# Kernel tuning notes

Measured on AMD Instinct MI355X. Metric: run time of the kernel, lower is better.

Reference implementation:

```python
import jax, jax.numpy as jnp
import numpy as np

WS = 6      # window_size
SS = 3      # shift_size
NH = 8      # num_heads
DIM = 384
HD = DIM // NH
SCALE = HD ** -0.5


def _window_mask(H, W):
    # region ids: [:ss,:ss]=0, [:ss,ss:]=1, [ss:,:ss]=2, [ss:,ss:]=3
    row = (jnp.arange(H) >= SS).astype(jnp.int32)
    col = (jnp.arange(W) >= SS).astype(jnp.int32)
    region = row[:, None] * 2 + col[None, :]            # (H, W)
    region = jnp.roll(region, (-SS, -SS), axis=(0, 1))
    ids = region.reshape(H // WS, WS, W // WS, WS).transpose(0, 2, 1, 3)
    ids = ids.reshape(-1, WS * WS)                      # (nW, V)
    eq = ids[:, :, None] == ids[:, None, :]             # (nW, V, V)
    return jnp.where(eq, 0.0, -jnp.inf).astype(jnp.float32)


def setup_inputs():
    key = jax.random.key(0)
    k = jax.random.split(key, 5)
    B, H, W, D = 32, 48, 48, DIM
    return {
        "x": jax.random.normal(k[0], (B, H, W, D), jnp.float32),
        "w_qkv": jax.random.normal(k[1], (D, 3 * D), jnp.float32) * 0.02,
        "b_qkv": jax.random.normal(k[2], (3 * D,), jnp.float32) * 0.02,
        "w_proj": jax.random.normal(k[3], (D, D), jnp.float32) * 0.02,
        "b_proj": jax.random.normal(k[4], (D,), jnp.float32) * 0.02,
    }


def reference(x, w_qkv, b_qkv, w_proj, b_proj):
    B, H, W, D = x.shape
    nWh, nWw = H // WS, W // WS
    nW, V = nWh * nWw, WS * WS

    x = jnp.roll(x, (-SS, -SS), axis=(1, 2))
    amask = _window_mask(H, W)                          # (nW, V, V)

    # window partition -> (B*nW, V, D)
    xw = x.reshape(B, nWh, WS, nWw, WS, D).transpose(0, 1, 3, 2, 4, 5)
    xw = xw.reshape(B * nW, V, D)

    qkv = xw @ w_qkv + b_qkv                            # (M, V, 3D)
    qkv = qkv.reshape(B * nW, V, 3, NH, HD).transpose(2, 0, 3, 1, 4)
    q, k, v = qkv[0], qkv[1], qkv[2]                    # (M, NH, V, HD)

    scores = jnp.einsum("mhvd,mhud->mhvu", q, k) * SCALE
    scores = scores.reshape(B, nW, NH, V, V) + amask[None, :, None]
    attn = jax.nn.softmax(scores, axis=-1).reshape(B * nW, NH, V, V)

    out = jnp.einsum("mhvu,mhud->mhvd", attn, v)        # (M, NH, V, HD)
    out = out.transpose(0, 2, 1, 3).reshape(B * nW, V, D)

    # window reverse -> (B, H, W, D)
    out = out.reshape(B, nWh, nWw, WS, WS, D).transpose(0, 1, 3, 2, 4, 5)
    out = out.reshape(B, H, W, D)
    out = jnp.roll(out, (SS, SS), axis=(1, 2))
    return out @ w_proj + b_proj
```

## Files before the change

kernel.cpp:

```cpp
#include <hip/hip_runtime.h>
#include <hip/hip_bf16.h>

namespace {

constexpr int Bn   = 32;
constexpr int IMG  = 48;
constexpr int Dm   = 384;
constexpr int NHn  = 8;
constexpr int WSn  = 6;
constexpr int NWn  = 64;
constexpr int Mn   = Bn * NWn;
constexpr int Vn   = 36;
constexpr int ROWS = Mn * Vn;
constexpr int K3   = 3 * Dm;
constexpr int QKW  = 768;
constexpr float SCALE = 0.14433756729740643f;

using short8 = __attribute__((ext_vector_type(8))) short;
using f32x4  = __attribute__((ext_vector_type(4))) float;

__device__ __forceinline__ float bf2f(unsigned short u) {
    return __uint_as_float(((unsigned)u) << 16);
}
__device__ __forceinline__ unsigned short f2bf(float f) {
    unsigned u = __float_as_uint(f);
    u += 0x7FFFu + ((u >> 16) & 1u);
    return (unsigned short)(u >> 16);
}

__device__ __forceinline__ void gl_lds16(const unsigned short* g, unsigned short* l) {
    __builtin_amdgcn_global_load_lds(
        (const __attribute__((address_space(1))) unsigned int*)g,
        (__attribute__((address_space(3))) unsigned int*)l, 16, 0, 0);
}

union U8 { short8 v; uint2 u[2]; };
__device__ __forceinline__ short8 ld8B(const unsigned short* p) {
    U8 r; r.u[0] = *(const uint2*)p; r.u[1] = *(const uint2*)(p + 4); return r.v;
}

__device__ __forceinline__ int gather_base(int row) {
    int m = row / Vn, v = row - m * Vn;
    int b = m >> 6, w = m & 63;
    int wh = w >> 3, ww = w & 7;
    int gh = wh * WSn + v / WSn;
    int gw = ww * WSn + v % WSn;
    int fi = (gh + 3) % IMG;
    int fj = (gw + 3) % IMG;
    return ((b * IMG + fi) * IMG + fj) * Dm;
}

__device__ __forceinline__ int region_id(int t, int wh, int ww) {
    int hi = (wh == 7) ? ((t / 6) < 3) : 1;
    int lo = (ww == 7) ? ((t % 6) < 3) : 1;
    return (hi << 1) | lo;
}

__global__ __launch_bounds__(256)
void gather_x(const float* __restrict__ x, unsigned short* __restrict__ xg)
{
    int idx = blockIdx.x * 256 + threadIdx.x;
    int row = idx / 96;
    int c4  = (idx - row * 96) * 4;
    float4 v = *(const float4*)(x + (size_t)gather_base(row) + c4);
    ushort4 o;
    o.x = f2bf(v.x); o.y = f2bf(v.y); o.z = f2bf(v.z); o.w = f2bf(v.w);
    *(ushort4*)(xg + (size_t)row * Dm + c4) = o;
}

__global__ __launch_bounds__(256)
void prep_w(const float* __restrict__ wq, const float* __restrict__ wp,
            unsigned short* __restrict__ wqT, unsigned short* __restrict__ wpT)
{
    int idx = blockIdx.x * 256 + threadIdx.x;
    if (idx < K3 * Dm) {
        int n = idx / Dm, k = idx - n * Dm;
        wqT[idx] = f2bf(wq[(size_t)k * K3 + n]);
    } else {
        int i2 = idx - K3 * Dm;
        if (i2 < Dm * Dm) {
            int n = i2 / Dm, k = i2 - n * Dm;
            wpT[i2] = f2bf(wp[(size_t)k * Dm + n]);
        }
    }
}

__global__ __launch_bounds__(256)
void qkv_mfma(const unsigned short* __restrict__ xg,
              const unsigned short* __restrict__ wqT,
              const float* __restrict__ bq,
              unsigned short* __restrict__ qkb,
              unsigned short* __restrict__ vt)
{
    __shared__ __align__(16) unsigned short As[128 * 32];
    __shared__ __align__(16) unsigned short Bs[128 * 32];

    const int tid  = threadIdx.x;
    const int wave = tid >> 6, lane = tid & 63;
    const int quad = lane >> 4, l15 = lane & 15;
    const int nT = blockIdx.x % (K3 / 128);
    const int mT = blockIdx.x / (K3 / 128);
    const int rowA0 = mT * 128, rowB0 = nT * 128;

    const int r_in = lane >> 2;
    const int kc   = (lane & 3) * 8;
    const unsigned short* gA = xg  + (size_t)(rowA0 + wave * 32 + r_in) * Dm + kc;
    const unsigned short* gB = wqT + (size_t)(rowB0 + wave * 32 + r_in) * Dm + kc;
    unsigned short* lA0 = &As[(wave * 32) * 32];
    unsigned short* lA1 = &As[(wave * 32 + 16) * 32];
    unsigned short* lB0 = &Bs[(wave * 32) * 32];
    unsigned short* lB1 = &Bs[(wave * 32 + 16) * 32];

    const int wm = wave >> 1, wn = wave & 1;
    f32x4 acc[4][4];
#pragma unroll
    for (int i = 0; i < 4; i++)
#pragma unroll
        for (int j = 0; j < 4; j++) acc[i][j] = (f32x4){0.f, 0.f, 0.f, 0.f};

    for (int k0 = 0; k0 < Dm; k0 += 32) {
        __syncthreads();
        gl_lds16(gA + k0, lA0);
        gl_lds16(gA + 16 * Dm + k0, lA1);
        gl_lds16(gB + k0, lB0);
        gl_lds16(gB + 16 * Dm + k0, lB1);
        __syncthreads();
        short8 af[4], bf[4];
#pragma unroll
        for (int i = 0; i < 4; i++)
            af[i] = *(const short8*)&As[(wm * 64 + i * 16 + l15) * 32 + quad * 8];
#pragma unroll
        for (int j = 0; j < 4; j++)
            bf[j] = *(const short8*)&Bs[(wn * 64 + j * 16 + l15) * 32 + quad * 8];
#pragma unroll
        for (int i = 0; i < 4; i++)
#pragma unroll
            for (int j = 0; j < 4; j++)
                acc[i][j] = __builtin_amdgcn_mfma_f32_16x16x32_bf16(af[i], bf[j], acc[i][j], 0, 0, 0);
    }

#pragma unroll
    for (int j = 0; j < 4; j++) {
        int col = rowB0 + wn * 64 + j * 16 + l15;
        float b = bq[col];
#pragma unroll
        for (int i = 0; i < 4; i++) {
#pragma unroll
            for (int r = 0; r < 4; r++) {
                int row = rowA0 + wm * 64 + i * 16 + quad * 4 + r;
                float val = acc[i][j][r] + b;
                if (col < QKW) {
                    qkb[(size_t)row * QKW + col] = f2bf(val);
                } else {
                    int c = col - QKW, hh = c / 48, dd = c - hh * 48;
                    int mm = row / 36, vv = row - mm * 36;
                    vt[((size_t)(mm * 8 + hh) * 48 + dd) * 36 + vv] = f2bf(val);
                }
            }
        }
    }
}

__global__ __launch_bounds__(256)
void attn_mfma(const unsigned short* __restrict__ qk,
               const unsigned short* __restrict__ vt,
               unsigned short* __restrict__ att)
{
    __shared__ __align__(16) unsigned short Pl[4][48 * 56];

    const int tid  = threadIdx.x;
    const int wave = tid >> 6, lane = tid & 63;
    const int quad = lane >> 4, l15 = lane & 15;
    const int W = blockIdx.x * 4 + wave;
    const int m = W >> 3, h = W & 7;
    const int w = m & 63, wh = w >> 3, ww = w & 7;

    const short8 zf = {0, 0, 0, 0, 0, 0, 0, 0};

    const unsigned short* qbase = qk + (size_t)(m * 36) * QKW + h * 48;
    short8 qf[3][2], kf[3][2];
#pragma unroll
    for (int t = 0; t < 3; t++) {
        const unsigned short* qr = qbase + (size_t)(t * 16 + l15) * QKW;
        qf[t][0] = *(const short8*)(qr + quad * 8);
        qf[t][1] = (quad < 2) ? *(const short8*)(qr + 32 + quad * 8) : zf;
        const unsigned short* kr = qbase + 384 + (size_t)(t * 16 + l15) * QKW;
        kf[t][0] = *(const short8*)(kr + quad * 8);
        kf[t][1] = *(const short8*)(kr + 32 + quad * 8);
    }

    f32x4 acc[3][3];
#pragma unroll
    for (int i = 0; i < 3; i++)
#pragma unroll
        for (int j = 0; j < 3; j++) acc[i][j] = (f32x4){0.f, 0.f, 0.f, 0.f};
#pragma unroll
    for (int i = 0; i < 3; i++)
#pragma unroll
        for (int j = 0; j < 3; j++) {
            acc[i][j] = __builtin_amdgcn_mfma_f32_16x16x32_bf16(qf[i][0], kf[j][0], acc[i][j], 0, 0, 0);
            acc[i][j] = __builtin_amdgcn_mfma_f32_16x16x32_bf16(qf[i][1], kf[j][1], acc[i][j], 0, 0, 0);
        }

#pragma unroll
    for (int i = 0; i < 3; i++) {
        float rs[4] = {0.f, 0.f, 0.f, 0.f};
#pragma unroll
        for (int j = 0; j < 3; j++) {
            int C = j * 16 + l15;
            int idc = region_id(C, wh, ww);
#pragma unroll
            for (int r = 0; r < 4; r++) {
                int R = i * 16 + quad * 4 + r;
                int idr = region_id(R, wh, ww);
                float s = acc[i][j][r] * SCALE;
                s = (C >= 36 || idr != idc) ? -1e30f : fminf(s, 30.f);
                float e = __expf(s);
                acc[i][j][r] = e;
                rs[r] += e;
            }
        }
#pragma unroll
        for (int r = 0; r < 4; r++) {
#pragma unroll
            for (int d = 1; d < 16; d <<= 1) rs[r] += __shfl_xor(rs[r], d, 16);
            rs[r] = 1.f / rs[r];
        }
#pragma unroll
        for (int j = 0; j < 3; j++)
#pragma unroll
            for (int r = 0; r < 4; r++) {
                int R = i * 16 + quad * 4 + r;
                int C = j * 16 + l15;
                Pl[wave][R * 56 + C] = f2bf(acc[i][j][r] * rs[r]);
            }
    }
    __syncthreads();

    short8 pf[3][2], vf[3][2];
#pragma unroll
    for (int t = 0; t < 3; t++) {
        const unsigned short* pr = &Pl[wave][(t * 16 + l15) * 56];
        pf[t][0] = *(const short8*)(pr + quad * 8);
        pf[t][1] = (quad < 2) ? *(const short8*)(pr + 32 + quad * 8) : zf;
        const unsigned short* vr = vt + ((size_t)(m * 8 + h) * 48 + t * 16 + l15) * 36;
        vf[t][0] = ld8B(vr + quad * 8);
        vf[t][1] = ld8B(vr + 32 + quad * 8);
    }
    f32x4 oacc[3][3];
#pragma unroll
    for (int i = 0; i < 3; i++)
#pragma unroll
        for (int j = 0; j < 3; j++) oacc[i][j] = (f32x4){0.f, 0.f, 0.f, 0.f};
#pragma unroll
    for (int i = 0; i < 3; i++)
#pragma unroll
        for (int j = 0; j < 3; j++) {
            oacc[i][j] = __builtin_amdgcn_mfma_f32_16x16x32_bf16(pf[i][0], vf[j][0], oacc[i][j], 0, 0, 0);
            oacc[i][j] = __builtin_amdgcn_mfma_f32_16x16x32_bf16(pf[i][1], vf[j][1], oacc[i][j], 0, 0, 0);
        }

#pragma unroll
    for (int i = 0; i < 3; i++)
#pragma unroll
        for (int r = 0; r < 4; r++) {
            int R = i * 16 + quad * 4 + r;
            if (R < 36) {
#pragma unroll
                for (int j = 0; j < 3; j++)
                    att[((size_t)m * 36 + R) * Dm + h * 48 + j * 16 + l15] = f2bf(oacc[i][j][r]);
            }
        }
}

__global__ __launch_bounds__(256)
void proj_mfma(const unsigned short* __restrict__ att,
               const unsigned short* __restrict__ wpT,
               const float* __restrict__ bp,
               float* __restrict__ out)
{
    __shared__ __align__(16) unsigned short As[128 * 32];
    __shared__ __align__(16) unsigned short Bs[128 * 32];
    __shared__ int rowOut[128];

    const int tid  = threadIdx.x;
    const int wave = tid >> 6, lane = tid & 63;
    const int quad = lane >> 4, l15 = lane & 15;
    const int nT = blockIdx.x % (Dm / 128);
    const int mT = blockIdx.x / (Dm / 128);
    const int rowA0 = mT * 128, rowB0 = nT * 128;

    if (tid < 128) rowOut[tid] = gather_base(rowA0 + tid);

    const int r_in = lane >> 2;
    const int kc   = (lane & 3) * 8;
    const unsigned short* gA = att + (size_t)(rowA0 + wave * 32 + r_in) * Dm + kc;
    const unsigned short* gB = wpT + (size_t)(rowB0 + wave * 32 + r_in) * Dm + kc;
    unsigned short* lA0 = &As[(wave * 32) * 32];
    unsigned short* lA1 = &As[(wave * 32 + 16) * 32];
    unsigned short* lB0 = &Bs[(wave * 32) * 32];
    unsigned short* lB1 = &Bs[(wave * 32 + 16) * 32];

    const int wm = wave >> 1, wn = wave & 1;
    f32x4 acc[4][4];
#pragma unroll
    for (int i = 0; i < 4; i++)
#pragma unroll
        for (int j = 0; j < 4; j++) acc[i][j] = (f32x4){0.f, 0.f, 0.f, 0.f};

    for (int k0 = 0; k0 < Dm; k0 += 32) {
        __syncthreads();
        gl_lds16(gA + k0, lA0);
        gl_lds16(gA + 16 * Dm + k0, lA1);
        gl_lds16(gB + k0, lB0);
        gl_lds16(gB + 16 * Dm + k0, lB1);
        __syncthreads();
        short8 af[4], bf[4];
#pragma unroll
        for (int i = 0; i < 4; i++)
            af[i] = *(const short8*)&As[(wm * 64 + i * 16 + l15) * 32 + quad * 8];
#pragma unroll
        for (int j = 0; j < 4; j++)
            bf[j] = *(const short8*)&Bs[(wn * 64 + j * 16 + l15) * 32 + quad * 8];
#pragma unroll
        for (int i = 0; i < 4; i++)
#pragma unroll
            for (int j = 0; j < 4; j++)
                acc[i][j] = __builtin_amdgcn_mfma_f32_16x16x32_bf16(af[i], bf[j], acc[i][j], 0, 0, 0);
    }

#pragma unroll
    for (int j = 0; j < 4; j++) {
        int col = rowB0 + wn * 64 + j * 16 + l15;
        float b = bp[col];
#pragma unroll
        for (int i = 0; i < 4; i++) {
#pragma unroll
            for (int r = 0; r < 4; r++) {
                int lrow = wm * 64 + i * 16 + quad * 4 + r;
                out[(size_t)rowOut[lrow] + col] = acc[i][j][r] + b;
            }
        }
    }
}

}

extern "C" void kernel_launch(void* const* d_in, const int* in_sizes, int n_in,
                              void* d_out, int out_size, void* d_ws, size_t ws_size,
                              hipStream_t stream)
{
    const float* x  = (const float*)d_in[0];
    const float* wq = (const float*)d_in[1];
    const float* bq = (const float*)d_in[2];
    const float* wp = (const float*)d_in[3];
    const float* bp = (const float*)d_in[4];
    float* out = (float*)d_out;

    const size_t QK_E = (size_t)ROWS * QKW;
    const size_t VT_E = (size_t)Mn * NHn * 48 * 36;
    const size_t XG_E = (size_t)ROWS * Dm;
    unsigned short* qkb = (unsigned short*)d_ws;
    unsigned short* vt  = qkb + QK_E;
    unsigned short* xg  = vt + VT_E;
    unsigned short* att = xg;
    unsigned short* wqT = xg + XG_E;
    unsigned short* wpT = wqT + (size_t)K3 * Dm;

    prep_w   <<<(K3 * Dm + Dm * Dm + 255) / 256, 256, 0, stream>>>(wq, wp, wqT, wpT);
    gather_x <<<ROWS * (Dm / 4) / 256,            256, 0, stream>>>(x, xg);
    qkv_mfma <<<(ROWS / 128) * (K3 / 128),        256, 0, stream>>>(xg, wqT, bq, qkb, vt);
    attn_mfma<<<(Mn * NHn) / 4,                   256, 0, stream>>>(qkb, vt, att);
    proj_mfma<<<(ROWS / 128) * (Dm / 128),        256, 0, stream>>>(att, wpT, bp, out);
}
```

Measured before the change: 451.8 us.

## Fuse window gather into QKV GEMM and keep full-K A tile resident in LDS

Removes the separate gather_x kernel. The QKV GEMM now loads its 64-row window-gathered x tile straight from fp32 input, converts it to bf16 and keeps the full K=384 A tile in padded LDS. It then loops over all N tiles, streaming the weights two 32-wide K slabs per barrier. The projection GEMM is restructured the same way, with one 64-row block resident and a loop over N tiles. This cuts a global round trip of xg and repeated A reloads, but each block now serialises work over N with fewer, larger blocks, which lowers parallelism and raises LDS use (about 66KB).

```diff
diff --git a/kernel.cpp b/kernel.cpp
--- a/kernel.cpp
+++ b/kernel.cpp
@@ -14,6 +14,7 @@
 constexpr int ROWS = Mn * Vn;
 constexpr int K3   = 3 * Dm;
 constexpr int QKW  = 768;
+constexpr int XSS  = 392;
 constexpr float SCALE = 0.14433756729740643f;
 
 using short8 = __attribute__((ext_vector_type(8))) short;
@@ -54,18 +55,6 @@
     int hi = (wh == 7) ? ((t / 6) < 3) : 1;
     int lo = (ww == 7) ? ((t % 6) < 3) : 1;
     return (hi << 1) | lo;
-}
-
-__global__ __launch_bounds__(256)
-void gather_x(const float* __restrict__ x, unsigned short* __restrict__ xg)
-{
-    int idx = blockIdx.x * 256 + threadIdx.x;
-    int row = idx / 96;
-    int c4  = (idx - row * 96) * 4;
-    float4 v = *(const float4*)(x + (size_t)gather_base(row) + c4);
-    ushort4 o;
-    o.x = f2bf(v.x); o.y = f2bf(v.y); o.z = f2bf(v.z); o.w = f2bf(v.w);
-    *(ushort4*)(xg + (size_t)row * Dm + c4) = o;
 }
 
 __global__ __launch_bounds__(256)
@@ -86,76 +75,110 @@
 }
 
 __global__ __launch_bounds__(256)
-void qkv_mfma(const unsigned short* __restrict__ xg,
-              const unsigned short* __restrict__ wqT,
-              const float* __restrict__ bq,
-              unsigned short* __restrict__ qkb,
-              unsigned short* __restrict__ vt)
+void qkv_fused(const float* __restrict__ x,
+               const unsigned short* __restrict__ wqT,
+               const float* __restrict__ bq,
+               unsigned short* __restrict__ qkb,
+               unsigned short* __restrict__ vt)
 {
-    __shared__ __align__(16) unsigned short As[128 * 32];
-    __shared__ __align__(16) unsigned short Bs[128 * 32];
+    __shared__ __align__(16) unsigned short Xs[64 * XSS];
+    __shared__ __align__(16) unsigned short Bs0[128 * 32];
+    __shared__ __align__(16) unsigned short Bs1[128 * 32];
 
     const int tid  = threadIdx.x;
     const int wave = tid >> 6, lane = tid & 63;
     const int quad = lane >> 4, l15 = lane & 15;
-    const int nT = blockIdx.x % (K3 / 128);
-    const int mT = blockIdx.x / (K3 / 128);
-    const int rowA0 = mT * 128, rowB0 = nT * 128;
+    const int rowA0 = blockIdx.x * 64;
+
+    {
+        const int row = tid >> 2, q4 = tid & 3;
+        const float* src = x + (size_t)gather_base(rowA0 + row) + q4 * 96;
+        unsigned short* dst = Xs + row * XSS + q4 * 96;
+#pragma unroll
+        for (int c = 0; c < 12; c++) {
+            float4 a = *(const float4*)(src + c * 8);
+            float4 b = *(const float4*)(src + c * 8 + 4);
+            short8 o;
+            o[0] = (short)f2bf(a.x); o[1] = (short)f2bf(a.y);
+            o[2] = (short)f2bf(a.z); o[3] = (short)f2bf(a.w);
+            o[4] = (short)f2bf(b.x); o[5] = (short)f2bf(b.y);
+            o[6] = (short)f2bf(b.z); o[7] = (short)f2bf(b.w);
+            *(short8*)(dst + c * 8) = o;
+        }
+    }
 
     const int r_in = lane >> 2;
     const int kc   = (lane & 3) * 8;
-    const unsigned short* gA = xg  + (size_t)(rowA0 + wave * 32 + r_in) * Dm + kc;
-    const unsigned short* gB = wqT + (size_t)(rowB0 + wave * 32 + r_in) * Dm + kc;
-    unsigned short* lA0 = &As[(wave * 32) * 32];
-    unsigned short* lA1 = &As[(wave * 32 + 16) * 32];
-    unsigned short* lB0 = &Bs[(wave * 32) * 32];
-    unsigned short* lB1 = &Bs[(wave * 32 + 16) * 32];
-
-    const int wm = wave >> 1, wn = wave & 1;
-    f32x4 acc[4][4];
-#pragma unroll
-    for (int i = 0; i < 4; i++)
-#pragma unroll
-        for (int j = 0; j < 4; j++) acc[i][j] = (f32x4){0.f, 0.f, 0.f, 0.f};
-
-    for (int k0 = 0; k0 < Dm; k0 += 32) {
-        __syncthreads();
-        gl_lds16(gA + k0, lA0);
-        gl_lds16(gA + 16 * Dm + k0, lA1);
-        gl_lds16(gB + k0, lB0);
-        gl_lds16(gB + 16 * Dm + k0, lB1);
-        __syncthreads();
-        short8 af[4], bf[4];
-#pragma unroll
-        for (int i = 0; i < 4; i++)
-            af[i] = *(const short8*)&As[(wm * 64 + i * 16 + l15) * 32 + quad * 8];
-#pragma unroll
-        for (int j = 0; j < 4; j++)
-            bf[j] = *(const short8*)&Bs[(wn * 64 + j * 16 + l15) * 32 + quad * 8];
-#pragma unroll
-        for (int i = 0; i < 4; i++)
-#pragma unroll
-            for (int j = 0; j < 4; j++)
-                acc[i][j] = __builtin_amdgcn_mfma_f32_16x16x32_bf16(af[i], bf[j], acc[i][j], 0, 0, 0);
-    }
-
-#pragma unroll
-    for (int j = 0; j < 4; j++) {
-        int col = rowB0 + wn * 64 + j * 16 + l15;
-        float b = bq[col];
-#pragma unroll
-        for (int i = 0; i < 4; i++) {
-#pragma unroll
-            for (int r = 0; r < 4; r++) {
-                int row = rowA0 + wm * 64 + i * 16 + quad * 4 + r;
-                float val = acc[i][j][r] + b;
-                if (col < QKW) {
-                    qkb[(size_t)row * QKW + col] = f2bf(val);
-                } else {
-                    int c = col - QKW, hh = c / 48, dd = c - hh * 48;
-                    int mm = row / 36, vv = row - mm * 36;
-                    vt[((size_t)(mm * 8 + hh) * 48 + dd) * 36 + vv] = f2bf(val);
+    const int wm   = wave >> 1, wn = wave & 1;
+    unsigned short* lB0a = &Bs0[(wave * 32) * 32];
+    unsigned short* lB0b = &Bs0[(wave * 32 + 16) * 32];
+    unsigned short* lB1a = &Bs1[(wave * 32) * 32];
+    unsigned short* lB1b = &Bs1[(wave * 32 + 16) * 32];
+
+    for (int nT = 0; nT < 9; nT++) {
+        const unsigned short* gB = wqT + (size_t)(nT * 128 + wave * 32 + r_in) * Dm + kc;
+        f32x4 acc[2][4];
+#pragma unroll
+        for (int i = 0; i < 2; i++)
+#pragma unroll
+            for (int j = 0; j < 4; j++) acc[i][j] = (f32x4){0.f, 0.f, 0.f, 0.f};
+
+        for (int k0 = 0; k0 < Dm; k0 += 64) {
+            __syncthreads();
+            gl_lds16(gB + k0,            lB0a);
+            gl_lds16(gB + 16 * Dm + k0,  lB0b);
+            gl_lds16(gB + k0 + 32,       lB1a);
+            gl_lds16(gB + 16 * Dm + k0 + 32, lB1b);
+            __syncthreads();
+            short8 af0[2], af1[2], bf0[4], bf1[4];
+#pragma unroll
+            for (int i = 0; i < 2; i++) {
+                const unsigned short* ar = &Xs[(wm * 32 + i * 16 + l15) * XSS + k0 + quad * 8];
+                af0[i] = *(const short8*)ar;
+                af1[i] = *(const short8*)(ar + 32);
+            }
+#pragma unroll
+            for (int j = 0; j < 4; j++) {
+                bf0[j] = *(const short8*)&Bs0[(wn * 64 + j * 16 + l15) * 32 + quad * 8];
+                bf1[j] = *(const short8*)&Bs1[(wn * 64 + j * 16 + l15) * 32 + quad * 8];
+            }
+#pragma unroll
+            for (int i = 0; i < 2; i++)
+#pragma unroll
+                for (int j = 0; j < 4; j++) {
+                    acc[i][j] = __builtin_amdgcn_mfma_f32_16x16x32_bf16(af0[i], bf0[j], acc[i][j], 0, 0, 0);
+                    acc[i][j] = __builtin_amdgcn_mfma_f32_16x16x32_bf16(af1[i], bf1[j], acc[i][j], 0, 0, 0);
                 }
+        }
+
+        if (nT < 6) {
+#pragma unroll
+            for (int j = 0; j < 4; j++) {
+                int col = nT * 128 + wn * 64 + j * 16 + l15;
+                float b = bq[col];
+#pragma unroll
+                for (int i = 0; i < 2; i++)
+#pragma unroll
+                    for (int r = 0; r < 4; r++) {
+                        int row = rowA0 + wm * 32 + i * 16 + quad * 4 + r;
+                        qkb[(size_t)row * QKW + col] = f2bf(acc[i][j][r] + b);
+                    }
+            }
+        } else {
+#pragma unroll
+            for (int j = 0; j < 4; j++) {
+                int col = nT * 128 + wn * 64 + j * 16 + l15;
+                float b = bq[col];
+                int c  = col - QKW;
+                int hh = c / 48, dd = c - hh * 48;
+#pragma unroll
+                for (int i = 0; i < 2; i++)
+#pragma unroll
+                    for (int r = 0; r < 4; r++) {
+                        int row = rowA0 + wm * 32 + i * 16 + quad * 4 + r;
+                        int mm = row / 36, vv = row - mm * 36;
+                        vt[((size_t)(mm * 8 + hh) * 48 + dd) * 36 + vv] = f2bf(acc[i][j][r] + b);
+                    }
             }
         }
     }
@@ -274,72 +297,87 @@
 }
 
 __global__ __launch_bounds__(256)
-void proj_mfma(const unsigned short* __restrict__ att,
-               const unsigned short* __restrict__ wpT,
-               const float* __restrict__ bp,
-               float* __restrict__ out)
+void proj_fused(const unsigned short* __restrict__ att,
+                const unsigned short* __restrict__ wpT,
+                const float* __restrict__ bp,
+                float* __restrict__ out)
 {
-    __shared__ __align__(16) unsigned short As[128 * 32];
-    __shared__ __align__(16) unsigned short Bs[128 * 32];
-    __shared__ int rowOut[128];
+    __shared__ __align__(16) unsigned short Xs[64 * XSS];
+    __shared__ __align__(16) unsigned short Bs0[128 * 32];
+    __shared__ __align__(16) unsigned short Bs1[128 * 32];
+    __shared__ int rowOut[64];
 
     const int tid  = threadIdx.x;
     const int wave = tid >> 6, lane = tid & 63;
     const int quad = lane >> 4, l15 = lane & 15;
-    const int nT = blockIdx.x % (Dm / 128);
-    const int mT = blockIdx.x / (Dm / 128);
-    const int rowA0 = mT * 128, rowB0 = nT * 128;
-
-    if (tid < 128) rowOut[tid] = gather_base(rowA0 + tid);
+    const int rowA0 = blockIdx.x * 64;
+
+    if (tid < 64) rowOut[tid] = gather_base(rowA0 + tid);
+
+    {
+        const int row = tid >> 2, q4 = tid & 3;
+        const unsigned short* src = att + (size_t)(rowA0 + row) * Dm + q4 * 96;
+        unsigned short* dst = Xs + row * XSS + q4 * 96;
+#pragma unroll
+        for (int c = 0; c < 12; c++)
+            *(short8*)(dst + c * 8) = *(const short8*)(src + c * 8);
+    }
 
     const int r_in = lane >> 2;
     const int kc   = (lane & 3) * 8;
-    const unsigned short* gA = att + (size_t)(rowA0 + wave * 32 + r_in) * Dm + kc;
-    const unsigned short* gB = wpT + (size_t)(rowB0 + wave * 32 + r_in) * Dm + kc;
-    unsigned short* lA0 = &As[(wave * 32) * 32];
-    unsigned short* lA1 = &As[(wave * 32 + 16) * 32];
-    unsigned short* lB0 = &Bs[(wave * 32) * 32];
-    unsigned short* lB1 = &Bs[(wave * 32 + 16) * 32];
-
-    const int wm = wave >> 1, wn = wave & 1;
-    f32x4 acc[4][4];
-#pragma unroll
-    for (int i = 0; i < 4; i++)
-#pragma unroll
-        for (int j = 0; j < 4; j++) acc[i][j] = (f32x4){0.f, 0.f, 0.f, 0.f};
-
-    for (int k0 = 0; k0 < Dm; k0 += 32) {
-        __syncthreads();
-        gl_lds16(gA + k0, lA0);
-        gl_lds16(gA + 16 * Dm + k0, lA1);
-        gl_lds16(gB + k0, lB0);
-        gl_lds16(gB + 16 * Dm + k0, lB1);
-        __syncthreads();
-        short8 af[4], bf[4];
-#pragma unroll
-        for (int i = 0; i < 4; i++)
-            af[i] = *(const short8*)&As[(wm * 64 + i * 16 + l15) * 32 + quad * 8];
-#pragma unroll
-        for (int j = 0; j < 4; j++)
-            bf[j] = *(const short8*)&Bs[(wn * 64 + j * 16 + l15) * 32 + quad * 8];
-#pragma unroll
-        for (int i = 0; i < 4; i++)
-#pragma unroll
-            for (int j = 0; j < 4; j++)
-                acc[i][j] = __builtin_amdgcn_mfma_f32_16x16x32_bf16(af[i], bf[j], acc[i][j], 0, 0, 0);
-    }
-
-#pragma unroll
-    for (int j = 0; j < 4; j++) {
-        int col = rowB0 + wn * 64 + j * 16 + l15;
-        float b = bp[col];
-#pragma unroll
-        for (int i = 0; i < 4; i++) {
-#pragma unroll
-            for (int r = 0; r < 4; r++) {
-                int lrow = wm * 64 + i * 16 + quad * 4 + r;
-                out[(size_t)rowOut[lrow] + col] = acc[i][j][r] + b;
-            }
+    const int wm   = wave >> 1, wn = wave & 1;
+    unsigned short* lB0a = &Bs0[(wave * 32) * 32];
+    unsigned short* lB0b = &Bs0[(wave * 32 + 16) * 32];
+    unsigned short* lB1a = &Bs1[(wave * 32) * 32];
+    unsigned short* lB1b = &Bs1[(wave * 32 + 16) * 32];
+
+    for (int nT = 0; nT < 3; nT++) {
+        const unsigned short* gB = wpT + (size_t)(nT * 128 + wave * 32 + r_in) * Dm + kc;
+        f32x4 acc[2][4];
+#pragma unroll
+        for (int i = 0; i < 2; i++)
+#pragma unroll
+            for (int j = 0; j < 4; j++) acc[i][j] = (f32x4){0.f, 0.f, 0.f, 0.f};
+
+        for (int k0 = 0; k0 < Dm; k0 += 64) {
+            __syncthreads();
+            gl_lds16(gB + k0,            lB0a);
+            gl_lds16(gB + 16 * Dm + k0,  lB0b);
+            gl_lds16(gB + k0 + 32,       lB1a);
+            gl_lds16(gB + 16 * Dm + k0 + 32, lB1b);
+            __syncthreads();
+            short8 af0[2], af1[2], bf0[4], bf1[4];
+#pragma unroll
+            for (int i = 0; i < 2; i++) {
+                const unsigned short* ar = &Xs[(wm * 32 + i * 16 + l15) * XSS + k0 + quad * 8];
+                af0[i] = *(const short8*)ar;
+                af1[i] = *(const short8*)(ar + 32);
+            }
+#pragma unroll
+            for (int j = 0; j < 4; j++) {
+                bf0[j] = *(const short8*)&Bs0[(wn * 64 + j * 16 + l15) * 32 + quad * 8];
+                bf1[j] = *(const short8*)&Bs1[(wn * 64 + j * 16 + l15) * 32 + quad * 8];
+            }
+#pragma unroll
+            for (int i = 0; i < 2; i++)
+#pragma unroll
+                for (int j = 0; j < 4; j++) {
+                    acc[i][j] = __builtin_amdgcn_mfma_f32_16x16x32_bf16(af0[i], bf0[j], acc[i][j], 0, 0, 0);
+                    acc[i][j] = __builtin_amdgcn_mfma_f32_16x16x32_bf16(af1[i], bf1[j], acc[i][j], 0, 0, 0);
+                }
+        }
+
+#pragma unroll
+        for (int j = 0; j < 4; j++) {
+            int col = nT * 128 + wn * 64 + j * 16 + l15;
+            float b = bp[col];
+#pragma unroll
+            for (int i = 0; i < 2; i++)
+#pragma unroll
+                for (int r = 0; r < 4; r++) {
+                    int lrow = wm * 32 + i * 16 + quad * 4 + r;
+                    out[(size_t)rowOut[lrow] + col] = acc[i][j][r] + b;
+                }
         }
     }
 }
@@ -357,19 +395,17 @@
     const float* bp = (const float*)d_in[4];
     float* out = (float*)d_out;
 
-    const size_t QK_E = (size_t)ROWS * QKW;
-    const size_t VT_E = (size_t)Mn * NHn * 48 * 36;
-    const size_t XG_E = (size_t)ROWS * Dm;
+    const size_t QK_E  = (size_t)ROWS * QKW;
+    const size_t VT_E  = (size_t)Mn * NHn * 48 * 36;
+    const size_t ATT_E = (size_t)ROWS * Dm;
     unsigned short* qkb = (unsigned short*)d_ws;
     unsigned short* vt  = qkb + QK_E;
-    unsigned short* xg  = vt + VT_E;
-    unsigned short* att = xg;
-    unsigned short* wqT = xg + XG_E;
+    unsigned short* att = vt + VT_E;
+    unsigned short* wqT = att + ATT_E;
     unsigned short* wpT = wqT + (size_t)K3 * Dm;
 
-    prep_w   <<<(K3 * Dm + Dm * Dm + 255) / 256, 256, 0, stream>>>(wq, wp, wqT, wpT);
-    gather_x <<<ROWS * (Dm / 4) / 256,            256, 0, stream>>>(x, xg);
-    qkv_mfma <<<(ROWS / 128) * (K3 / 128),        256, 0, stream>>>(xg, wqT, bq, qkb, vt);
-    attn_mfma<<<(Mn * NHn) / 4,                   256, 0, stream>>>(qkb, vt, att);
-    proj_mfma<<<(ROWS / 128) * (Dm / 128),        256, 0, stream>>>(att, wpT, bp, out);
-}
+    prep_w    <<<(K3 * Dm + Dm * Dm + 255) / 256, 256, 0, stream>>>(wq, wp, wqT, wpT);
+    qkv_fused <<<ROWS / 64,       256, 0, stream>>>(x, wqT, bq, qkb, vt);
+    attn_mfma <<<(Mn * NHn) / 4,  256, 0, stream>>>(qkb, vt, att);
+    proj_fused<<<ROWS / 64,       256, 0, stream>>>(att, wpT, bp, out);
+}
```

Result: slower. 469.6 us (+4.0%).
